# Optimization experiments

Measured on AMD Instinct MI355X. Metric: run time of the kernel, lower is better.

## Reference

```python
import jax, jax.numpy as jnp
import numpy as np

D_MODEL = 768
N_HEAD = 12
D_K = D_MODEL // N_HEAD
B, S = 2, 2048


def setup_inputs() -> dict:
    key = jax.random.key(0)
    ks = jax.random.split(key, 13)
    scale = 1.0 / np.sqrt(D_MODEL)
    inp = {
        'q': jax.random.normal(ks[0], (B, S, D_MODEL), jnp.float32),
        'k': jax.random.normal(ks[1], (B, S, D_MODEL), jnp.float32),
        'v': jax.random.normal(ks[2], (B, S, D_MODEL), jnp.float32),
        'Wq': jax.random.normal(ks[3], (D_MODEL, D_MODEL), jnp.float32) * scale,
        'bq': jnp.zeros((D_MODEL,), jnp.float32),
        'Wk': jax.random.normal(ks[4], (D_MODEL, D_MODEL), jnp.float32) * scale,
        'bk': jnp.zeros((D_MODEL,), jnp.float32),
        'Wv': jax.random.normal(ks[5], (D_MODEL, D_MODEL), jnp.float32) * scale,
        'bv': jnp.zeros((D_MODEL,), jnp.float32),
        'Wo': jax.random.normal(ks[6], (D_MODEL, D_MODEL), jnp.float32) * scale,
        'bo': jnp.zeros((D_MODEL,), jnp.float32),
        'mask': jax.random.randint(ks[7], (B, 1, S), 0, 2, jnp.int32),
    }
    return inp


def reference(q, k, v, Wq, bq, Wk, bk, Wv, bv, Wo, bo, mask):
    # project and split heads: [B,S,D] -> [B,H,S,Dk]
    def heads(x, W, b):
        y = x @ W + b
        return y.reshape(B, S, N_HEAD, D_K).transpose(0, 2, 1, 3)

    qh = heads(q, Wq, bq)
    kh = heads(k, Wk, bk)
    vh = heads(v, Wv, bv)
    # full score matrix [B,H,S,S] (intentionally materialized, as in source)
    scores = jnp.einsum('bhqd,bhkd->bhqk', qh, kh) / jnp.sqrt(jnp.float32(D_K))
    m = mask[:, None, :, :]  # [B,1,1,S] broadcast over heads and queries
    scores = jnp.where(m == 0, jnp.float32(-1e9), scores)
    p_attn = jax.nn.softmax(scores, axis=-1)
    # dropout omitted (eval / deterministic reference)
    x = jnp.einsum('bhqk,bhkd->bhqd', p_attn, vh)
    x = x.transpose(0, 2, 1, 3).reshape(B, S, D_MODEL)
    return x @ Wo + bo
```

## Files before the change

kernel.cpp:

```cpp
#include <hip/hip_runtime.h>


#define H_ 12
#define DK_ 64
#define B_DIM 2
#define SEQ 2048
#define DM 768
#define MROWS 4096
#define PER_IN ((size_t)MROWS * DM)
#define QSCALE 0.18033688011112042f

typedef short bf16x8 __attribute__((ext_vector_type(8)));
typedef short bf16x4 __attribute__((ext_vector_type(4)));
typedef float f32x4 __attribute__((ext_vector_type(4)));
typedef float f32x16 __attribute__((ext_vector_type(16)));

__device__ inline unsigned short f2bf(float f) {
    union { float f; unsigned int i; } x; x.f = f;
    unsigned int r = x.i + 0x7fff + ((x.i >> 16) & 1);
    return (unsigned short)(r >> 16);
}

__device__ inline unsigned pack2bf(float lo, float hi) {
#if __has_builtin(__builtin_amdgcn_cvt_pk_bf16_f32)
    auto v = __builtin_amdgcn_cvt_pk_bf16_f32(lo, hi);
    return __builtin_bit_cast(unsigned, v);
#else
    return (unsigned)f2bf(lo) | ((unsigned)f2bf(hi) << 16);
#endif
}

__device__ inline float exp2fast(float x) {
#if __has_builtin(__builtin_amdgcn_exp2f)
    return __builtin_amdgcn_exp2f(x);
#else
    return exp2f(x);
#endif
}

__device__ inline f32x16 mfma32x8(bf16x4 a, bf16x4 b, f32x16 c) {
#if __has_builtin(__builtin_amdgcn_mfma_f32_32x32x8bf16_1k)
    return __builtin_amdgcn_mfma_f32_32x32x8bf16_1k(a, b, c, 0, 0, 0);
#else
    asm("v_mfma_f32_32x32x8_bf16 %0, %1, %2, %0" : "+v"(c) : "v"(a), "v"(b));
    return c;
#endif
}

__device__ inline void gload_lds16(const unsigned short* g, unsigned short* ldsbase,
                                   int lane) {
#if __has_builtin(__builtin_amdgcn_global_load_lds)
    __builtin_amdgcn_global_load_lds(
        (const __attribute__((address_space(1))) unsigned int*)g,
        (__attribute__((address_space(3))) unsigned int*)ldsbase, 16, 0, 0);
#else
    *(uint4*)(ldsbase + 8 * lane) = *(const uint4*)g;
#endif
}

__global__ void cvt3(const float* __restrict__ a, const float* __restrict__ b,
                     const float* __restrict__ c,
                     unsigned short* __restrict__ oa, unsigned short* __restrict__ ob,
                     unsigned short* __restrict__ oc) {
    const float* src = blockIdx.y == 0 ? a : (blockIdx.y == 1 ? b : c);
    unsigned short* dst = blockIdx.y == 0 ? oa : (blockIdx.y == 1 ? ob : oc);
    size_t i = ((size_t)blockIdx.x * 256 + threadIdx.x) * 4;
    float4 f = *(const float4*)(src + i);
    ushort4 u;
    u.x = f2bf(f.x); u.y = f2bf(f.y); u.z = f2bf(f.z); u.w = f2bf(f.w);
    *(ushort4*)(dst + i) = u;
}

__global__ void transpose4(const float* __restrict__ w0, const float* __restrict__ w1,
                           const float* __restrict__ w2, const float* __restrict__ w3,
                           unsigned short* __restrict__ outbase) {
    const float* in = blockIdx.z == 0 ? w0 : (blockIdx.z == 1 ? w1 : (blockIdx.z == 2 ? w2 : w3));
    unsigned short* out = outbase + (size_t)blockIdx.z * DM * DM;
    __shared__ unsigned short t[32][33];
    int x = threadIdx.x, y = threadIdx.y;
    int k0 = blockIdx.x * 32, n0 = blockIdx.y * 32;
#pragma unroll
    for (int i = 0; i < 32; i += 8)
        t[y + i][x] = f2bf(in[(size_t)(k0 + y + i) * DM + n0 + x]);
    __syncthreads();
#pragma unroll
    for (int i = 0; i < 32; i += 8)
        out[(size_t)(n0 + y + i) * DM + k0 + x] = t[x][y + i];
}

__global__ __launch_bounds__(256) void maskscan(const int* __restrict__ mask,
                                                int* __restrict__ idx,
                                                int* __restrict__ nkeys) {
    __shared__ int wsum[4];
    int b = blockIdx.x, tid = threadIdx.x;
    int lane = tid & 63, wave = tid >> 6;
    const int* mp = mask + (size_t)b * SEQ + tid * 8;
    int4 a = *(const int4*)mp;
    int4 c = *(const int4*)(mp + 4);
    int m[8] = {a.x, a.y, a.z, a.w, c.x, c.y, c.z, c.w};
    int pre[8], s = 0;
#pragma unroll
    for (int e = 0; e < 8; e++) { pre[e] = s; s += (m[e] != 0); }
    int incl = s;
#pragma unroll
    for (int off = 1; off < 64; off <<= 1) {
        int v = __shfl_up(incl, off);
        if (lane >= off) incl += v;
    }
    int lexcl = incl - s;
    if (lane == 63) wsum[wave] = incl;
    __syncthreads();
    int base = lexcl;
    for (int w = 0; w < wave; w++) base += wsum[w];
#pragma unroll
    for (int e = 0; e < 8; e++)
        if (m[e]) idx[b * SEQ + base + pre[e]] = tid * 8 + e;
    if (tid == 0) nkeys[b] = wsum[0] + wsum[1] + wsum[2] + wsum[3];
}

__global__ __launch_bounds__(256) void gatherKV(const unsigned short* __restrict__ Kh,
                                                const unsigned short* __restrict__ Vn,
                                                const int* __restrict__ idx,
                                                const int* __restrict__ nkeys,
                                                unsigned short* __restrict__ Kc,
                                                unsigned short* __restrict__ Vtc) {
    __shared__ unsigned short Tl[64][72];
    int tid = threadIdx.x;
    int j0 = blockIdx.x * 64, bh = blockIdx.y, b = bh / H_;
    int n = nkeys[b];
    int row = tid >> 2, cb = (tid & 3) * 16;
    int j = j0 + row;
    int src = j < n ? idx[b * SEQ + j] : -1;
    unsigned short v[16];
    unsigned short* ok = Kc + ((size_t)bh * SEQ + j) * DK_ + cb;
    if (src >= 0) {
        const unsigned short* gv = Vn + ((size_t)bh * SEQ + src) * DK_ + cb;
        *(uint4*)&v[0] = *(const uint4*)gv;
        *(uint4*)&v[8] = *(const uint4*)(gv + 8);
        const unsigned short* gk = Kh + ((size_t)bh * SEQ + src) * DK_ + cb;
        uint4 k0 = *(const uint4*)gk;
        uint4 k1 = *(const uint4*)(gk + 8);
        *(uint4*)ok = k0;
        *(uint4*)(ok + 8) = k1;
    } else {
        uint4 z = {0u, 0u, 0u, 0u};
        *(uint4*)&v[0] = z;
        *(uint4*)&v[8] = z;
        *(uint4*)ok = z;
        *(uint4*)(ok + 8) = z;
    }
#pragma unroll
    for (int e = 0; e < 16; e++)
        Tl[cb + e][row] = v[e];
    __syncthreads();
    uint4 o0 = *(const uint4*)&Tl[row][cb];
    uint4 o1 = *(const uint4*)&Tl[row][cb + 8];
    unsigned short* out = Vtc + ((size_t)bh * DK_ + row) * SEQ + j0 + cb;
    *(uint4*)out = o0;
    *(uint4*)(out + 8) = o1;
}

template <int QKV>
__global__ __launch_bounds__(256) void gemm128(
    const unsigned short* __restrict__ A0, const unsigned short* __restrict__ A1,
    const unsigned short* __restrict__ A2, const unsigned short* __restrict__ Wt,
    const float* __restrict__ bias0, const float* __restrict__ bias1,
    const float* __restrict__ bias2,
    void* __restrict__ O0, void* __restrict__ O1, void* __restrict__ O2) {
    __shared__ unsigned short S[2][128][64];
    unsigned short (*Al)[64] = S[0];
    unsigned short (*Bl)[64] = S[1];
    const int K = DM;
    int tid = threadIdx.x;
    int wave = tid >> 6, lane = tid & 63, quad = lane >> 4, l15 = lane & 15;
    int wr = wave >> 1, wc = wave & 1;
    int m0 = blockIdx.x * 128, n0 = blockIdx.y * 128;
    int lrow = lane >> 3, lcol = (lane & 7) * 8;

    int mi = 0, nb0 = n0;
    const unsigned short* A = A0;
    const float* bias = bias0;
    void* O = O0;
    if constexpr (QKV) {
        mi = n0 >= 1536 ? 2 : (n0 >= 768 ? 1 : 0);
        nb0 = n0 - mi * 768;
        A = mi == 0 ? A0 : (mi == 1 ? A1 : A2);
        bias = mi == 0 ? bias0 : (mi == 1 ? bias1 : bias2);
        O = mi == 0 ? O0 : (mi == 1 ? O1 : O2);
    }

    f32x4 acc[4][4];
#pragma unroll
    for (int i = 0; i < 4; i++)
#pragma unroll
        for (int j = 0; j < 4; j++)
#pragma unroll
            for (int r = 0; r < 4; r++) acc[i][j][r] = 0.f;

    const unsigned short* gA = A + (size_t)(m0 + 32 * wave + lrow) * K + lcol;
    const unsigned short* gB = Wt + (size_t)(n0 + 32 * wave + lrow) * K + lcol;

    for (int k0 = 0; k0 < K; k0 += 64) {
        __syncthreads();
#pragma unroll
        for (int c = 0; c < 4; c++) {
            gload_lds16(gA + (size_t)8 * c * K + k0, &Al[32 * wave + 8 * c][0], lane);
            gload_lds16(gB + (size_t)8 * c * K + k0, &Bl[32 * wave + 8 * c][0], lane);
        }
        __syncthreads();
#pragma unroll
        for (int ks = 0; ks < 64; ks += 32) {
            bf16x8 af[4], bfr[4];
#pragma unroll
            for (int i = 0; i < 4; i++)
                af[i] = *(const bf16x8*)&Al[64 * wr + 16 * i + l15][ks + 8 * quad];
#pragma unroll
            for (int j = 0; j < 4; j++)
                bfr[j] = *(const bf16x8*)&Bl[64 * wc + 16 * j + l15][ks + 8 * quad];
#pragma unroll
            for (int i = 0; i < 4; i++)
#pragma unroll
                for (int j = 0; j < 4; j++)
                    acc[i][j] = __builtin_amdgcn_mfma_f32_16x16x32_bf16(af[i], bfr[j], acc[i][j], 0, 0, 0);
        }
    }

    if constexpr (!QKV) {
#pragma unroll
        for (int j = 0; j < 4; j++) {
            int nn = nb0 + 64 * wc + 16 * j + l15;
            float bv = bias[nn];
#pragma unroll
            for (int i = 0; i < 4; i++)
#pragma unroll
                for (int r = 0; r < 4; r++) {
                    int m = m0 + 64 * wr + 16 * i + 4 * quad + r;
                    ((float*)O0)[(size_t)m * DM + nn] = acc[i][j][r] + bv;
                }
        }
    } else {
        float sc = mi == 0 ? QSCALE : 1.0f;
        __syncthreads();
        unsigned short (*Cl)[128] = (unsigned short(*)[128])S;
#pragma unroll
        for (int j = 0; j < 4; j++) {
            float bv = bias[nb0 + 64 * wc + 16 * j + l15];
#pragma unroll
            for (int i = 0; i < 4; i++)
#pragma unroll
                for (int r = 0; r < 4; r++)
                    Cl[64 * wr + 16 * i + 4 * quad + r][64 * wc + 16 * j + l15] =
                        f2bf((acc[i][j][r] + bv) * sc);
        }
        __syncthreads();
        int row = tid >> 1, half = tid & 1;
        int m = m0 + row;
        int b = m >> 11, s = m & 2047;
        int h = (nb0 + 64 * half) >> 6;
        unsigned short* og = (unsigned short*)O + ((size_t)(b * H_ + h) * SEQ + s) * DK_;
        const unsigned short* cr = &Cl[row][64 * half];
#pragma unroll
        for (int c = 0; c < 4; c++)
            *(uint4*)(og + 16 * c) = *(const uint4*)(cr + 16 * c);
#pragma unroll
        for (int c = 0; c < 4; c++)
            *(uint4*)(og + 16 * c + 8) = *(const uint4*)(cr + 16 * c + 8);
    }
}

__global__ __launch_bounds__(256) void attn_fa(const unsigned short* __restrict__ Q,
                                               const unsigned short* __restrict__ Kc,
                                               const unsigned short* __restrict__ Vtc,
                                               const int* __restrict__ nkeys,
                                               unsigned short* __restrict__ ctx) {
    __shared__ __align__(16) unsigned short Ql[64][72];
    __shared__ __align__(16) unsigned short Kl[64][72];
    __shared__ __align__(16) unsigned short Vl[64][68];
    __shared__ __align__(16) float Op[2][32][32];
    __shared__ __align__(16) float lp[2][32];
    int tid = threadIdx.x;
    int wave = tid >> 6, lane = tid & 63;
    int l31 = lane & 31, hi = lane >> 5;
    int qh = wave & 1, kh = wave >> 1;
    int bh = blockIdx.y, b = bh / H_, h = bh % H_;
    int q0 = blockIdx.x * 64;

    int n = nkeys[b];
    int nt = (n + 63) >> 6;
    float padf = (float)(nt * 64 - n);

    {
        int row = tid >> 2, cb = (tid & 3) * 16;
        const unsigned short* gq = Q + ((size_t)bh * SEQ + q0 + row) * DK_ + cb;
        *(uint4*)&Ql[row][cb]     = *(const uint4*)gq;
        *(uint4*)&Ql[row][cb + 8] = *(const uint4*)(gq + 8);
    }
    __syncthreads();

    bf16x8 qf[4];
#pragma unroll
    for (int c = 0; c < 4; c++)
        qf[c] = *(const bf16x8*)&Ql[32 * qh + l31][16 * c + 8 * hi];

    float lrow = 0.f;
    f32x16 o[2][2];
#pragma unroll
    for (int dt = 0; dt < 2; dt++)
#pragma unroll
        for (int p = 0; p < 2; p++)
#pragma unroll
            for (int r = 0; r < 16; r++) o[dt][p][r] = 0.f;

    int krow = tid >> 2, kcb = (tid & 3) * 16;
    const unsigned short* gk = Kc + ((size_t)bh * SEQ + krow) * DK_ + kcb;
    const unsigned short* gv = Vtc + ((size_t)bh * DK_ + krow) * SEQ + kcb;

    uint4 kr0 = *(const uint4*)gk, kr1 = *(const uint4*)(gk + 8);
    uint4 vr0 = *(const uint4*)gv, vr1 = *(const uint4*)(gv + 8);

    for (int kt = 0; kt < nt; kt++) {
        __syncthreads();
        *(uint4*)&Kl[krow][kcb]     = kr0;
        *(uint4*)&Kl[krow][kcb + 8] = kr1;
        *(uint4*)&Vl[krow][kcb]     = vr0;
        *(uint4*)&Vl[krow][kcb + 8] = vr1;
        __syncthreads();
        if (kt + 1 < nt) {
            gk += (size_t)64 * DK_;
            gv += 64;
            kr0 = *(const uint4*)gk; kr1 = *(const uint4*)(gk + 8);
            vr0 = *(const uint4*)gv; vr1 = *(const uint4*)(gv + 8);
        }

        f32x16 sT;
#pragma unroll
        for (int r = 0; r < 16; r++) sT[r] = 0.f;
#pragma unroll
        for (int c = 0; c < 4; c++) {
            bf16x8 kf = *(const bf16x8*)&Kl[32 * kh + l31][16 * c + 8 * hi];
            sT = __builtin_amdgcn_mfma_f32_32x32x16_bf16(kf, qf[c], sT, 0, 0, 0);
        }

        bf16x4 pfrag[4];
#pragma unroll
        for (int c = 0; c < 4; c++) {
            float p0 = exp2fast(sT[4 * c + 0]);
            float p1 = exp2fast(sT[4 * c + 1]);
            float p2 = exp2fast(sT[4 * c + 2]);
            float p3 = exp2fast(sT[4 * c + 3]);
            lrow += (p0 + p1) + (p2 + p3);
            union { unsigned u[2]; bf16x4 v; } pk;
            pk.u[0] = pack2bf(p0, p1);
            pk.u[1] = pack2bf(p2, p3);
            pfrag[c] = pk.v;
        }

#pragma unroll
        for (int dt = 0; dt < 2; dt++)
#pragma unroll
            for (int c = 0; c < 4; c++) {
                bf16x4 vf = *(const bf16x4*)&Vl[32 * dt + l31][32 * kh + 8 * c + 4 * hi];
                o[dt][c & 1] = mfma32x8(pfrag[c], vf, o[dt][c & 1]);
            }
    }

    lrow += __shfl_xor(lrow, 32);
    float inv = 0.f;
#pragma unroll
    for (int dt = 0; dt < 2; dt++) {
        if (kh == 1) {
#pragma unroll
            for (int r = 0; r < 16; r++) {
                int qrl = (r & 3) + 8 * (r >> 2) + 4 * hi;
                Op[qh][qrl][l31] = o[dt][0][r] + o[dt][1][r];
            }
            if (dt == 0 && hi == 0) lp[qh][l31] = lrow;
        }
        __syncthreads();
        if (kh == 0) {
            if (dt == 0) {
                float l = lrow + lp[qh][l31] - padf;
                inv = l > 0.f ? 1.f / l : 0.f;
            }
#pragma unroll
            for (int r = 0; r < 16; r++) {
                int qrl = (r & 3) + 8 * (r >> 2) + 4 * hi;
                float invr = __shfl(inv, qrl);
                int qg = q0 + 32 * qh + qrl;
                size_t base = ((size_t)b * SEQ + qg) * DM + h * DK_;
                float v = o[dt][0][r] + o[dt][1][r] + Op[qh][qrl][l31];
                ctx[base + 32 * dt + l31] = f2bf(v * invr);
            }
        }
        __syncthreads();
    }
}

extern "C" void kernel_launch(void* const* d_in, const int* in_sizes, int n_in,
                              void* d_out, int out_size, void* d_ws, size_t ws_size,
                              hipStream_t stream) {
    const float* q  = (const float*)d_in[0];
    const float* k  = (const float*)d_in[1];
    const float* v  = (const float*)d_in[2];
    const float* Wq = (const float*)d_in[3];
    const float* bq = (const float*)d_in[4];
    const float* Wk = (const float*)d_in[5];
    const float* bk = (const float*)d_in[6];
    const float* Wv = (const float*)d_in[7];
    const float* bv = (const float*)d_in[8];
    const float* Wo = (const float*)d_in[9];
    const float* bo = (const float*)d_in[10];
    const int* mask = (const int*)d_in[11];

    unsigned short* ws = (unsigned short*)d_ws;
    unsigned short* qb = ws;
    unsigned short* kb = ws + PER_IN;
    unsigned short* vb = ws + 2 * PER_IN;
    unsigned short* Qh = ws + 3 * PER_IN;
    unsigned short* Kh = ws + 4 * PER_IN;
    unsigned short* Vhn = ws + 5 * PER_IN;
    unsigned short* WtQKV = ws + 6 * PER_IN;
    unsigned short* WtO = WtQKV + (size_t)3 * DM * DM;
    unsigned short* Kc = kb;
    unsigned short* Vtc = vb;
    unsigned short* ctx = qb;
    int* idx = (int*)d_out;
    int* nk = idx + B_DIM * SEQ;

    cvt3<<<dim3(PER_IN / 1024, 3), 256, 0, stream>>>(q, k, v, qb, kb, vb);
    transpose4<<<dim3(DM / 32, DM / 32, 4), dim3(32, 8), 0, stream>>>(Wq, Wk, Wv, Wo, WtQKV);

    gemm128<1><<<dim3(MROWS / 128, 3 * DM / 128), 256, 0, stream>>>(
        qb, kb, vb, WtQKV, bq, bk, bv, Qh, Kh, Vhn);

    maskscan<<<dim3(B_DIM), 256, 0, stream>>>(mask, idx, nk);
    gatherKV<<<dim3(SEQ / 64, B_DIM * H_), 256, 0, stream>>>(Kh, Vhn, idx, nk, Kc, Vtc);

    attn_fa<<<dim3(SEQ / 64, B_DIM * H_), 256, 0, stream>>>(Qh, Kc, Vtc, nk, ctx);

    gemm128<0><<<dim3(MROWS / 128, DM / 128), 256, 0, stream>>>(
        ctx, ctx, ctx, WtO, bo, bo, bo, d_out, d_out, d_out);
}
```

Before: 212.4 us.

## Double-buffer LDS tiles in gemm128 to overlap global loads with MFMA

```diff
diff --git a/kernel.cpp b/kernel.cpp
--- a/kernel.cpp
+++ b/kernel.cpp
@@ -167,10 +167,9 @@
     const float* __restrict__ bias0, const float* __restrict__ bias1,
     const float* __restrict__ bias2,
     void* __restrict__ O0, void* __restrict__ O1, void* __restrict__ O2) {
-    __shared__ unsigned short S[2][128][64];
-    unsigned short (*Al)[64] = S[0];
-    unsigned short (*Bl)[64] = S[1];
+    __shared__ unsigned short S[2][2][128][64];
     const int K = DM;
+    const int NT = K / 64;
     int tid = threadIdx.x;
     int wave = tid >> 6, lane = tid & 63, quad = lane >> 4, l15 = lane & 15;
     int wr = wave >> 1, wc = wave & 1;
@@ -200,14 +199,29 @@
     const unsigned short* gA = A + (size_t)(m0 + 32 * wave + lrow) * K + lcol;
     const unsigned short* gB = Wt + (size_t)(n0 + 32 * wave + lrow) * K + lcol;
 
-    for (int k0 = 0; k0 < K; k0 += 64) {
-        __syncthreads();
-#pragma unroll
-        for (int c = 0; c < 4; c++) {
-            gload_lds16(gA + (size_t)8 * c * K + k0, &Al[32 * wave + 8 * c][0], lane);
-            gload_lds16(gB + (size_t)8 * c * K + k0, &Bl[32 * wave + 8 * c][0], lane);
-        }
-        __syncthreads();
+#pragma unroll
+    for (int c = 0; c < 4; c++) {
+        gload_lds16(gA + (size_t)8 * c * K, &S[0][0][32 * wave + 8 * c][0], lane);
+        gload_lds16(gB + (size_t)8 * c * K, &S[0][1][32 * wave + 8 * c][0], lane);
+    }
+
+    for (int t = 0; t < NT; t++) {
+        int cur = t & 1;
+        if (t + 1 < NT) {
+            int k0 = (t + 1) * 64;
+#pragma unroll
+            for (int c = 0; c < 4; c++) {
+                gload_lds16(gA + (size_t)8 * c * K + k0, &S[cur ^ 1][0][32 * wave + 8 * c][0], lane);
+                gload_lds16(gB + (size_t)8 * c * K + k0, &S[cur ^ 1][1][32 * wave + 8 * c][0], lane);
+            }
+            asm volatile("s_waitcnt vmcnt(8)" ::: "memory");
+        } else {
+            asm volatile("s_waitcnt vmcnt(0)" ::: "memory");
+        }
+        __builtin_amdgcn_s_barrier();
+
+        unsigned short (*Al)[64] = S[cur][0];
+        unsigned short (*Bl)[64] = S[cur][1];
 #pragma unroll
         for (int ks = 0; ks < 64; ks += 32) {
             bf16x8 af[4], bfr[4];
@@ -223,6 +237,8 @@
                 for (int j = 0; j < 4; j++)
                     acc[i][j] = __builtin_amdgcn_mfma_f32_16x16x32_bf16(af[i], bfr[j], acc[i][j], 0, 0, 0);
         }
+        asm volatile("" ::: "memory");
+        __builtin_amdgcn_s_barrier();
     }
 
     if constexpr (!QKV) {
```

New measurement: 199.0 us. -6.3%, faster.
